# Kernel optimization log

Hardware: AMD Instinct MI355X
Metric: run time of the kernel (lower is better)

Reference implementation:

```python
import jax, jax.numpy as jnp
import numpy as np

NUM_HEADS = 16
THRESHOLD = 4e-4  # < 1/S so every softmax row keeps >=1 entry (classical path of grover_search_filter)


def setup_inputs() -> dict:
    key = jax.random.key(0)
    k0, k1, k2 = jax.random.split(key, 3)
    B, S, E = 4, 1024, 1024
    x = jax.random.normal(k0, (B, S, E), dtype=jnp.float32)
    Wqkv = jax.random.normal(k1, (3 * E, E), dtype=jnp.float32) * 0.02
    bqkv = jnp.zeros((3 * E,), dtype=jnp.float32)
    Wproj = jax.random.normal(k2, (E, E), dtype=jnp.float32) * 0.02
    bproj = jnp.zeros((E,), dtype=jnp.float32)
    return {"x": x, "Wqkv": Wqkv, "bqkv": bqkv, "Wproj": Wproj, "bproj": bproj}


def reference(x, Wqkv, bqkv, Wproj, bproj):
    B, S, E = x.shape
    H = NUM_HEADS
    D = E // H
    scale = D ** -0.5
    # qkv projection -> (3, B, H, S, D), matching torch permute(2,0,3,1,4)
    qkv = (x @ Wqkv.T + bqkv).reshape(B, S, 3, H, D).transpose(2, 0, 3, 1, 4)
    q, k, v = qkv[0], qkv[1], qkv[2]
    attn_logits = jnp.einsum("bhqd,bhkd->bhqk", q, k) * scale  # [B,H,S,S]
    attn_probs = jax.nn.softmax(attn_logits, axis=-1)
    # grover_search_filter: seq_len > 2**max_qubits -> classical threshold mask
    selected = attn_probs > THRESHOLD
    filtered_logits = jnp.where(selected, attn_logits, -jnp.inf)
    filtered_attn = jax.nn.softmax(filtered_logits, axis=-1)
    # dropout is identity in eval mode
    out = jnp.einsum("bhqk,bhkd->bhqd", filtered_attn, v)
    out = out.transpose(0, 2, 1, 3).reshape(B, S, E)
    out = out @ Wproj.T + bproj
    return out, filtered_attn
```

## Files before the change

kernel.cpp:

```cpp
#include <hip/hip_runtime.h>
#include <hip/hip_bf16.h>
#include <cstdint>


#define BB 4
#define SS 1024
#define EE 1024
#define HH 16
#define DD 64

typedef __attribute__((ext_vector_type(8))) short bf16x8;
typedef __attribute__((ext_vector_type(4))) float f32x4;

__global__ __launch_bounds__(256) void split_f32(
    const float* __restrict__ in, __hip_bfloat16* __restrict__ hi,
    __hip_bfloat16* __restrict__ lo, int n4) {
  int i = blockIdx.x * 256 + threadIdx.x;
  if (i >= n4) return;
  float4 v = ((const float4*)in)[i];
  float vv[4] = {v.x, v.y, v.z, v.w};
  __hip_bfloat16 h[4], l[4];
#pragma unroll
  for (int j = 0; j < 4; ++j) {
    h[j] = __float2bfloat16(vv[j]);
    l[j] = __float2bfloat16(vv[j] - __bfloat162float(h[j]));
  }
  ((ushort4*)hi)[i] = *(ushort4*)h;
  if (lo) ((ushort4*)lo)[i] = *(ushort4*)l;
}

template <int MODE>
__global__ __launch_bounds__(256) void gemm(
    const __hip_bfloat16* __restrict__ Ah, const __hip_bfloat16* __restrict__ Al,
    const __hip_bfloat16* __restrict__ Bh, const __hip_bfloat16* __restrict__ Bl,
    const float* __restrict__ Af, const float* __restrict__ bias,
    float* __restrict__ oF, __hip_bfloat16* __restrict__ o1,
    __hip_bfloat16* __restrict__ o2, __hip_bfloat16* __restrict__ o3,
    __hip_bfloat16* __restrict__ o4, __hip_bfloat16* __restrict__ o5,
    int M, int N, int K, int lda, int ldb, long long sA, long long sB) {
  constexpr bool SPLIT = (MODE == 0 || MODE == 1);
  constexpr bool AF32  = (MODE == 2);

  const int tid  = threadIdx.x;
  const int lane = tid & 63;
  const int wave = tid >> 6;
  const int wm   = (wave >> 1) * 64;
  const int wn   = (wave & 1) * 64;
  const int quad = lane >> 4;
  const int l15  = lane & 15;
  const int m0   = blockIdx.y * 128;
  const int n0   = blockIdx.x * 128;
  const long long zz = blockIdx.z;

  if (AF32) Af += zz * sA;
  else { Ah += zz * sA; if (SPLIT) Al += zz * sA; }
  Bh += zz * sB;
  if (SPLIT) Bl += zz * sB;

  __shared__ __align__(16) __hip_bfloat16 lds[(SPLIT ? 4 : 2) * 128 * 72];
  __hip_bfloat16* lAh = lds;
  __hip_bfloat16* lAl = SPLIT ? lds + 128 * 72 : nullptr;
  __hip_bfloat16* lBh = lds + (SPLIT ? 2 : 1) * 128 * 72;
  __hip_bfloat16* lBl = SPLIT ? lds + 3 * 128 * 72 : nullptr;

  f32x4 acc[4][4] = {};

  for (int k0 = 0; k0 < K; k0 += 64) {
#pragma unroll
    for (int it = 0; it < 4; ++it) {
      int flat = (it * 256 + tid) * 8;
      int row  = flat >> 6;
      int kk   = flat & 63;
      const bool mok = (m0 + row < M);
      const bool nok = (n0 + row < N);
      if (AF32) {
        float4 f0 = {0, 0, 0, 0}, f1 = {0, 0, 0, 0};
        if (mok) {
          const float* src = Af + (long long)(m0 + row) * lda + k0 + kk;
          f0 = *(const float4*)src;
          f1 = *(const float4*)(src + 4);
        }
        __hip_bfloat16 t[8];
        t[0] = __float2bfloat16(f0.x); t[1] = __float2bfloat16(f0.y);
        t[2] = __float2bfloat16(f0.z); t[3] = __float2bfloat16(f0.w);
        t[4] = __float2bfloat16(f1.x); t[5] = __float2bfloat16(f1.y);
        t[6] = __float2bfloat16(f1.z); t[7] = __float2bfloat16(f1.w);
        *(uint4*)&lAh[row * 72 + kk] = *(uint4*)t;
      } else {
        uint4 va = {0, 0, 0, 0};
        if (mok) va = *(const uint4*)(Ah + (long long)(m0 + row) * lda + k0 + kk);
        *(uint4*)&lAh[row * 72 + kk] = va;
        if (SPLIT) {
          uint4 vl = {0, 0, 0, 0};
          if (mok) vl = *(const uint4*)(Al + (long long)(m0 + row) * lda + k0 + kk);
          *(uint4*)&lAl[row * 72 + kk] = vl;
        }
      }
      uint4 vb = {0, 0, 0, 0};
      if (nok) vb = *(const uint4*)(Bh + (long long)(n0 + row) * ldb + k0 + kk);
      *(uint4*)&lBh[row * 72 + kk] = vb;
      if (SPLIT) {
        uint4 vbl = {0, 0, 0, 0};
        if (nok) vbl = *(const uint4*)(Bl + (long long)(n0 + row) * ldb + k0 + kk);
        *(uint4*)&lBl[row * 72 + kk] = vbl;
      }
    }
    __syncthreads();

#pragma unroll
    for (int ks = 0; ks < 64; ks += 32) {
      bf16x8 ah[4], bh[4], al[4], bl[4];
#pragma unroll
      for (int i = 0; i < 4; ++i) {
        int off = (wm + i * 16 + l15) * 72 + ks + quad * 8;
        ah[i] = *(const bf16x8*)&lAh[off];
        if (SPLIT) al[i] = *(const bf16x8*)&lAl[off];
      }
#pragma unroll
      for (int j = 0; j < 4; ++j) {
        int off = (wn + j * 16 + l15) * 72 + ks + quad * 8;
        bh[j] = *(const bf16x8*)&lBh[off];
        if (SPLIT) bl[j] = *(const bf16x8*)&lBl[off];
      }
#pragma unroll
      for (int i = 0; i < 4; ++i)
#pragma unroll
        for (int j = 0; j < 4; ++j) {
          if (SPLIT) {
            acc[i][j] = __builtin_amdgcn_mfma_f32_16x16x32_bf16(al[i], bh[j], acc[i][j], 0, 0, 0);
            acc[i][j] = __builtin_amdgcn_mfma_f32_16x16x32_bf16(ah[i], bl[j], acc[i][j], 0, 0, 0);
          }
          acc[i][j] = __builtin_amdgcn_mfma_f32_16x16x32_bf16(ah[i], bh[j], acc[i][j], 0, 0, 0);
        }
    }
    __syncthreads();
  }

#pragma unroll
  for (int i = 0; i < 4; ++i) {
#pragma unroll
    for (int j = 0; j < 4; ++j) {
#pragma unroll
      for (int r = 0; r < 4; ++r) {
        int m = m0 + wm + i * 16 + quad * 4 + r;
        int n = n0 + wn + j * 16 + l15;
        float v = acc[i][j][r];
        if (MODE == 0) {
          v += bias[n];
          int c = n >> 10, nn = n & 1023, h = nn >> 6, d = nn & 63;
          int b = m >> 10, s = m & 1023;
          long long idx = (((long long)(b * HH + h) * SS + s) << 6) + d;
          if (c == 0) {
            __hip_bfloat16 hh = __float2bfloat16(v);
            o1[idx] = hh;
            o2[idx] = __float2bfloat16(v - __bfloat162float(hh));
          } else if (c == 1) {
            __hip_bfloat16 hh = __float2bfloat16(v);
            o3[idx] = hh;
            o4[idx] = __float2bfloat16(v - __bfloat162float(hh));
          } else {
            o5[(((long long)(b * HH + h) * DD + d) << 10) + s] = __float2bfloat16(v);
          }
        } else if (MODE == 1) {
          oF[zz * (SS * SS) + (long long)m * SS + n] = v * 0.125f;
        } else if (MODE == 2) {
          if (n < DD) {
            int b = (int)(zz >> 4), h = (int)(zz & 15);
            o1[(((long long)(b * SS + m)) << 10) + h * DD + n] = __float2bfloat16(v);
          }
        } else {
          oF[(long long)m * EE + n] = v + bias[n];
        }
      }
    }
  }
}

__device__ __forceinline__ float wave_max64(float v) {
#pragma unroll
  for (int o = 32; o > 0; o >>= 1) v = fmaxf(v, __shfl_xor(v, o));
  return v;
}
__device__ __forceinline__ float wave_sum64(float v) {
#pragma unroll
  for (int o = 32; o > 0; o >>= 1) v += __shfl_xor(v, o);
  return v;
}

__global__ __launch_bounds__(256) void softmax_filter(float* __restrict__ attn) {
  const int lane = threadIdx.x & 63;
  const long long row = (long long)blockIdx.x * 4 + (threadIdx.x >> 6);
  float* p = attn + (row << 10);

  float4 raw[4];
#pragma unroll
  for (int i = 0; i < 4; ++i) raw[i] = ((const float4*)p)[i * 64 + lane];
  float v[16];
#pragma unroll
  for (int i = 0; i < 4; ++i) {
    v[i * 4 + 0] = raw[i].x; v[i * 4 + 1] = raw[i].y;
    v[i * 4 + 2] = raw[i].z; v[i * 4 + 3] = raw[i].w;
  }

  float mloc = v[0];
#pragma unroll
  for (int t = 1; t < 16; ++t) mloc = fmaxf(mloc, v[t]);
  const float m = wave_max64(mloc);

  float e[16], zloc = 0.f;
#pragma unroll
  for (int t = 0; t < 16; ++t) { e[t] = expf(v[t] - m); zloc += e[t]; }
  const float Z = wave_sum64(zloc);

  float zsloc = 0.f;
  bool sel[16];
#pragma unroll
  for (int t = 0; t < 16; ++t) {
    sel[t] = (e[t] / Z) > 4e-4f;
    if (sel[t]) zsloc += e[t];
  }
  const float Zs = wave_sum64(zsloc);

#pragma unroll
  for (int i = 0; i < 4; ++i) {
    float4 w;
    w.x = sel[i * 4 + 0] ? e[i * 4 + 0] / Zs : 0.f;
    w.y = sel[i * 4 + 1] ? e[i * 4 + 1] / Zs : 0.f;
    w.z = sel[i * 4 + 2] ? e[i * 4 + 2] / Zs : 0.f;
    w.w = sel[i * 4 + 3] ? e[i * 4 + 3] / Zs : 0.f;
    ((float4*)p)[i * 64 + lane] = w;
  }
}

extern "C" void kernel_launch(void* const* d_in, const int* in_sizes, int n_in,
                              void* d_out, int out_size, void* d_ws, size_t ws_size,
                              hipStream_t stream) {
  const float* x     = (const float*)d_in[0];
  const float* Wqkv  = (const float*)d_in[1];
  const float* bqkv  = (const float*)d_in[2];
  const float* Wproj = (const float*)d_in[3];
  const float* bproj = (const float*)d_in[4];

  float* out   = (float*)d_out;
  float* attnF = out + (size_t)BB * SS * EE;

  const size_t M1 = 1024 * 1024;
  __hip_bfloat16* w = (__hip_bfloat16*)d_ws;

  if (ws_size >= (size_t)80 * 1024 * 1024) {
    __hip_bfloat16 *xh = w, *xl = xh + 4 * M1;
    __hip_bfloat16 *Wqh = xl + 4 * M1, *Wql = Wqh + 3 * M1, *Wph = Wql + 3 * M1;
    __hip_bfloat16 *qh = Wph + M1, *ql = qh + 4 * M1, *kh = ql + 4 * M1, *kl = kh + 4 * M1;
    __hip_bfloat16 *vT = kl + 4 * M1, *ao = vT + 4 * M1;

    split_f32<<<4096, 256, 0, stream>>>(x, xh, xl, 1024 * 1024);
    split_f32<<<3072, 256, 0, stream>>>(Wqkv, Wqh, Wql, 768 * 1024);
    split_f32<<<1024, 256, 0, stream>>>(Wproj, Wph, nullptr, 256 * 1024);

    gemm<0><<<dim3(24, 32, 1), 256, 0, stream>>>(
        xh, xl, Wqh, Wql, nullptr, bqkv, nullptr, qh, ql, kh, kl, vT,
        4096, 3072, 1024, 1024, 1024, 0LL, 0LL);
    gemm<1><<<dim3(8, 8, 64), 256, 0, stream>>>(
        qh, ql, kh, kl, nullptr, nullptr, attnF, nullptr, nullptr, nullptr, nullptr, nullptr,
        1024, 1024, 64, 64, 64, (long long)(SS * DD), (long long)(SS * DD));
    softmax_filter<<<dim3(65536 / 4), 256, 0, stream>>>(attnF);
    gemm<2><<<dim3(1, 8, 64), 256, 0, stream>>>(
        nullptr, nullptr, vT, nullptr, attnF, nullptr, nullptr, ao, nullptr, nullptr, nullptr, nullptr,
        1024, 64, 1024, 1024, 1024, (long long)(SS * SS), (long long)(DD * SS));
    gemm<3><<<dim3(8, 32, 1), 256, 0, stream>>>(
        ao, nullptr, Wph, nullptr, nullptr, bproj, out, nullptr, nullptr, nullptr, nullptr, nullptr,
        4096, 1024, 1024, 1024, 1024, 0LL, 0LL);
    return;
  }

  __hip_bfloat16 *Wqh = w, *Wql = Wqh + 3 * M1, *Wph = Wql + 3 * M1;
  __hip_bfloat16 *xh = Wph + M1, *xl = xh + M1;
  __hip_bfloat16 *qh = xl + M1, *ql = qh + M1, *kh = ql + M1, *kl = kh + M1;
  __hip_bfloat16 *vT = kl + M1, *ao = vT + M1;

  split_f32<<<3072, 256, 0, stream>>>(Wqkv, Wqh, Wql, 768 * 1024);
  split_f32<<<1024, 256, 0, stream>>>(Wproj, Wph, nullptr, 256 * 1024);

  for (int b = 0; b < BB; ++b) {
    const float* xb   = x + (size_t)b * SS * EE;
    float* attnb      = attnF + (size_t)b * HH * SS * SS;
    float* outb       = out + (size_t)b * SS * EE;

    split_f32<<<1024, 256, 0, stream>>>(xb, xh, xl, 256 * 1024);
    gemm<0><<<dim3(24, 8, 1), 256, 0, stream>>>(
        xh, xl, Wqh, Wql, nullptr, bqkv, nullptr, qh, ql, kh, kl, vT,
        1024, 3072, 1024, 1024, 1024, 0LL, 0LL);
    gemm<1><<<dim3(8, 8, 16), 256, 0, stream>>>(
        qh, ql, kh, kl, nullptr, nullptr, attnb, nullptr, nullptr, nullptr, nullptr, nullptr,
        1024, 1024, 64, 64, 64, (long long)(SS * DD), (long long)(SS * DD));
    softmax_filter<<<dim3(16384 / 4), 256, 0, stream>>>(attnb);
    gemm<2><<<dim3(1, 8, 16), 256, 0, stream>>>(
        nullptr, nullptr, vT, nullptr, attnb, nullptr, nullptr, ao, nullptr, nullptr, nullptr, nullptr,
        1024, 64, 1024, 1024, 1024, (long long)(SS * SS), (long long)(DD * SS));
    gemm<3><<<dim3(8, 8, 1), 256, 0, stream>>>(
        ao, nullptr, Wph, nullptr, nullptr, bproj, outb, nullptr, nullptr, nullptr, nullptr, nullptr,
        1024, 1024, 1024, 1024, 1024, 0LL, 0LL);
  }
}
```

Before: 751.1 us.

## Fuse QK^T, threshold softmax and PV into one attention kernel

Replaces the separate QK^T GEMM, in-place softmax-filter pass and PV GEMM with a single kernel per 16-query tile per head. Logits are held in LDS, softmax and filtering run there, and the probabilities are written once to the attention output and reused as bf16 from LDS for the PV MFMA. This removes the write-then-read round trip of the 256MB attention matrix and two launches. In exchange, each block reloads all K rows for only 16 queries, and the large LDS tile (about 66KB) limits occupancy.

```diff
diff --git a/kernel.cpp b/kernel.cpp
--- a/kernel.cpp
+++ b/kernel.cpp
@@ -187,48 +187,105 @@
   return v;
 }
 
-__global__ __launch_bounds__(256) void softmax_filter(float* __restrict__ attn) {
-  const int lane = threadIdx.x & 63;
-  const long long row = (long long)blockIdx.x * 4 + (threadIdx.x >> 6);
-  float* p = attn + (row << 10);
-
-  float4 raw[4];
-#pragma unroll
-  for (int i = 0; i < 4; ++i) raw[i] = ((const float4*)p)[i * 64 + lane];
-  float v[16];
-#pragma unroll
-  for (int i = 0; i < 4; ++i) {
-    v[i * 4 + 0] = raw[i].x; v[i * 4 + 1] = raw[i].y;
-    v[i * 4 + 2] = raw[i].z; v[i * 4 + 3] = raw[i].w;
-  }
-
-  float mloc = v[0];
-#pragma unroll
-  for (int t = 1; t < 16; ++t) mloc = fmaxf(mloc, v[t]);
-  const float m = wave_max64(mloc);
-
-  float e[16], zloc = 0.f;
-#pragma unroll
-  for (int t = 0; t < 16; ++t) { e[t] = expf(v[t] - m); zloc += e[t]; }
-  const float Z = wave_sum64(zloc);
-
-  float zsloc = 0.f;
-  bool sel[16];
-#pragma unroll
-  for (int t = 0; t < 16; ++t) {
-    sel[t] = (e[t] / Z) > 4e-4f;
-    if (sel[t]) zsloc += e[t];
-  }
-  const float Zs = wave_sum64(zsloc);
-
-#pragma unroll
-  for (int i = 0; i < 4; ++i) {
-    float4 w;
-    w.x = sel[i * 4 + 0] ? e[i * 4 + 0] / Zs : 0.f;
-    w.y = sel[i * 4 + 1] ? e[i * 4 + 1] / Zs : 0.f;
-    w.z = sel[i * 4 + 2] ? e[i * 4 + 2] / Zs : 0.f;
-    w.w = sel[i * 4 + 3] ? e[i * 4 + 3] / Zs : 0.f;
-    ((float4*)p)[i * 64 + lane] = w;
+__global__ __launch_bounds__(256) void fused_attn(
+    const __hip_bfloat16* __restrict__ qh, const __hip_bfloat16* __restrict__ ql,
+    const __hip_bfloat16* __restrict__ kh, const __hip_bfloat16* __restrict__ kl,
+    const __hip_bfloat16* __restrict__ vT, float* __restrict__ attn,
+    __hip_bfloat16* __restrict__ ao) {
+  const int tid  = threadIdx.x;
+  const int lane = tid & 63;
+  const int wave = tid >> 6;
+  const int quad = lane >> 4;
+  const int l15  = lane & 15;
+  const int bh   = blockIdx.y;
+  const int q0   = blockIdx.x * 16;
+  const int brow = (bh >> 4) * SS;
+  const int h    = bh & 15;
+  const long long qbase = ((long long)bh * SS + q0) * DD;
+  const long long kbase = (long long)bh * SS * DD;
+  const long long vbase = (long long)bh * DD * SS;
+  const long long abase = ((long long)bh * SS + q0) * SS;
+
+  __shared__ __align__(16) float lg[16][1032];
+
+  bf16x8 aqh[2], aql[2];
+  {
+    const __hip_bfloat16* ph = qh + qbase + l15 * DD + quad * 8;
+    const __hip_bfloat16* pl = ql + qbase + l15 * DD + quad * 8;
+    aqh[0] = *(const bf16x8*)(ph);
+    aqh[1] = *(const bf16x8*)(ph + 32);
+    aql[0] = *(const bf16x8*)(pl);
+    aql[1] = *(const bf16x8*)(pl + 32);
+  }
+
+#pragma unroll
+  for (int nt = 0; nt < 16; ++nt) {
+    const int n = wave * 256 + nt * 16;
+    const __hip_bfloat16* pkh = kh + kbase + (long long)(n + l15) * DD + quad * 8;
+    const __hip_bfloat16* pkl = kl + kbase + (long long)(n + l15) * DD + quad * 8;
+    bf16x8 bh0 = *(const bf16x8*)(pkh);
+    bf16x8 bh1 = *(const bf16x8*)(pkh + 32);
+    bf16x8 bl0 = *(const bf16x8*)(pkl);
+    bf16x8 bl1 = *(const bf16x8*)(pkl + 32);
+    f32x4 acc = {};
+    acc = __builtin_amdgcn_mfma_f32_16x16x32_bf16(aql[0], bh0, acc, 0, 0, 0);
+    acc = __builtin_amdgcn_mfma_f32_16x16x32_bf16(aqh[0], bl0, acc, 0, 0, 0);
+    acc = __builtin_amdgcn_mfma_f32_16x16x32_bf16(aqh[0], bh0, acc, 0, 0, 0);
+    acc = __builtin_amdgcn_mfma_f32_16x16x32_bf16(aql[1], bh1, acc, 0, 0, 0);
+    acc = __builtin_amdgcn_mfma_f32_16x16x32_bf16(aqh[1], bl1, acc, 0, 0, 0);
+    acc = __builtin_amdgcn_mfma_f32_16x16x32_bf16(aqh[1], bh1, acc, 0, 0, 0);
+#pragma unroll
+    for (int r = 0; r < 4; ++r) lg[quad * 4 + r][n + l15] = acc[r] * 0.125f;
+  }
+  __syncthreads();
+
+#pragma unroll
+  for (int rr = 0; rr < 4; ++rr) {
+    const int row = wave * 4 + rr;
+    float v[16];
+#pragma unroll
+    for (int i = 0; i < 16; ++i) v[i] = lg[row][lane + i * 64];
+    float mloc = v[0];
+#pragma unroll
+    for (int t = 1; t < 16; ++t) mloc = fmaxf(mloc, v[t]);
+    const float m = wave_max64(mloc);
+    float e[16], zloc = 0.f;
+#pragma unroll
+    for (int t = 0; t < 16; ++t) { e[t] = expf(v[t] - m); zloc += e[t]; }
+    const float Z = wave_sum64(zloc);
+    float zsloc = 0.f;
+    bool sel[16];
+#pragma unroll
+    for (int t = 0; t < 16; ++t) {
+      sel[t] = (e[t] / Z) > 4e-4f;
+      if (sel[t]) zsloc += e[t];
+    }
+    const float Zs = wave_sum64(zsloc);
+    float* arow = attn + abase + (long long)row * SS;
+    __hip_bfloat16* prow = (__hip_bfloat16*)&lg[row][0];
+#pragma unroll
+    for (int i = 0; i < 16; ++i) {
+      const float w = sel[i] ? e[i] / Zs : 0.f;
+      arow[lane + i * 64] = w;
+      prow[lane + i * 64] = __float2bfloat16(w);
+    }
+  }
+  __syncthreads();
+
+  const int d0 = wave * 16;
+  f32x4 oacc = {};
+  const __hip_bfloat16* pv = vT + vbase + (long long)(d0 + l15) * SS + quad * 8;
+  const __hip_bfloat16* pp = (const __hip_bfloat16*)&lg[l15][0] + quad * 8;
+#pragma unroll
+  for (int ks = 0; ks < 32; ++ks) {
+    bf16x8 ap = *(const bf16x8*)(pp + ks * 32);
+    bf16x8 bv = *(const bf16x8*)(pv + ks * 32);
+    oacc = __builtin_amdgcn_mfma_f32_16x16x32_bf16(ap, bv, oacc, 0, 0, 0);
+  }
+#pragma unroll
+  for (int r = 0; r < 4; ++r) {
+    const int q = q0 + quad * 4 + r;
+    ao[((long long)(brow + q)) * EE + h * DD + d0 + l15] = __float2bfloat16(oacc[r]);
   }
 }
 
@@ -260,13 +317,8 @@
     gemm<0><<<dim3(24, 32, 1), 256, 0, stream>>>(
         xh, xl, Wqh, Wql, nullptr, bqkv, nullptr, qh, ql, kh, kl, vT,
         4096, 3072, 1024, 1024, 1024, 0LL, 0LL);
-    gemm<1><<<dim3(8, 8, 64), 256, 0, stream>>>(
-        qh, ql, kh, kl, nullptr, nullptr, attnF, nullptr, nullptr, nullptr, nullptr, nullptr,
-        1024, 1024, 64, 64, 64, (long long)(SS * DD), (long long)(SS * DD));
-    softmax_filter<<<dim3(65536 / 4), 256, 0, stream>>>(attnF);
-    gemm<2><<<dim3(1, 8, 64), 256, 0, stream>>>(
-        nullptr, nullptr, vT, nullptr, attnF, nullptr, nullptr, ao, nullptr, nullptr, nullptr, nullptr,
-        1024, 64, 1024, 1024, 1024, (long long)(SS * SS), (long long)(DD * SS));
+    fused_attn<<<dim3(SS / 16, BB * HH), 256, 0, stream>>>(
+        qh, ql, kh, kl, vT, attnF, ao);
     gemm<3><<<dim3(8, 32, 1), 256, 0, stream>>>(
         ao, nullptr, Wph, nullptr, nullptr, bproj, out, nullptr, nullptr, nullptr, nullptr, nullptr,
         4096, 1024, 1024, 1024, 1024, 0LL, 0LL);
@@ -290,13 +342,8 @@
     gemm<0><<<dim3(24, 8, 1), 256, 0, stream>>>(
         xh, xl, Wqh, Wql, nullptr, bqkv, nullptr, qh, ql, kh, kl, vT,
         1024, 3072, 1024, 1024, 1024, 0LL, 0LL);
-    gemm<1><<<dim3(8, 8, 16), 256, 0, stream>>>(
-        qh, ql, kh, kl, nullptr, nullptr, attnb, nullptr, nullptr, nullptr, nullptr, nullptr,
-        1024, 1024, 64, 64, 64, (long long)(SS * DD), (long long)(SS * DD));
-    softmax_filter<<<dim3(16384 / 4), 256, 0, stream>>>(attnb);
-    gemm<2><<<dim3(1, 8, 16), 256, 0, stream>>>(
-        nullptr, nullptr, vT, nullptr, attnb, nullptr, nullptr, ao, nullptr, nullptr, nullptr, nullptr,
-        1024, 64, 1024, 1024, 1024, (long long)(SS * SS), (long long)(DD * SS));
+    fused_attn<<<dim3(SS / 16, HH), 256, 0, stream>>>(
+        qh, ql, kh, kl, vT, attnb, ao);
     gemm<3><<<dim3(8, 8, 1), 256, 0, stream>>>(
         ao, nullptr, Wph, nullptr, nullptr, bproj, outb, nullptr, nullptr, nullptr, nullptr, nullptr,
         1024, 1024, 1024, 1024, 1024, 0LL, 0LL);
```

After: 702.7 us. -6.4%, faster.
